# Kernel tuning notes

Hardware: AMD Instinct MI355X
Metric: run time of the kernel (lower is better)

The kernel has to match this reference:

```python
import jax, jax.numpy as jnp
import numpy as np

T, IN, H, OUT, L = 128, 64, 2048, 4096, 2  # steps, input_size, hidden, output vocab, layers


def lstm_cell(x, h, c, Wih, Whh, bih, bhh):
    # torch LSTMCell: gates = x W_ih^T + b_ih + h W_hh^T + b_hh; order i,f,g,o
    g = x @ Wih.T + bih + h @ Whh.T + bhh
    i, f, gg, o = jnp.split(g, 4, axis=-1)
    c_new = jax.nn.sigmoid(f) * c + jax.nn.sigmoid(i) * jnp.tanh(gg)
    h_new = jax.nn.sigmoid(o) * jnp.tanh(c_new)
    return h_new, c_new


def setup_inputs() -> dict:
    key = jax.random.key(0)
    ks = jax.random.split(key, 12)
    u = lambda k, shape, fan: jax.random.uniform(k, shape, jnp.float32, -1.0, 1.0) / np.sqrt(fan)
    return {
        "input": jax.random.normal(ks[0], (T, 1, IN), jnp.float32),
        "h0": jnp.zeros((L, 1, H), jnp.float32),
        "c0": jnp.zeros((L, 1, H), jnp.float32),
        "Wih0": u(ks[1], (4 * H, IN + 1), H),
        "Whh0": u(ks[2], (4 * H, H), H),
        "bih0": u(ks[3], (4 * H,), H),
        "bhh0": u(ks[4], (4 * H,), H),
        "Wih1": u(ks[5], (4 * H, H), H),
        "Whh1": u(ks[6], (4 * H, H), H),
        "bih1": u(ks[7], (4 * H,), H),
        "bhh1": u(ks[8], (4 * H,), H),
        "Wl": u(ks[9], (OUT, H), H),
        "bl": u(ks[10], (OUT,), H),
    }


def reference(input, h0, c0, Wih0, Whh0, bih0, bhh0, Wih1, Whh1, bih1, bhh1, Wl, bl):
    keys = jax.random.split(jax.random.key(42), input.shape[0])

    def step(carry, xs):
        prev, h, c = carry          # prev: [1,1] float (last sampled index, init 1.0)
        x_t, k = xs                 # x_t: [1, IN]
        xa = jnp.concatenate([prev, x_t], axis=1)  # [1, IN+1]
        h0n, c0n = lstm_cell(xa, h[0], c[0], Wih0, Whh0, bih0, bhh0)
        h1n, c1n = lstm_cell(h0n, h[1], c[1], Wih1, Whh1, bih1, bhh1)
        logits = h1n @ Wl.T + bl                    # [1, OUT]
        probs = jax.nn.softmax(logits, axis=-1)
        samp = jax.random.categorical(k, logits, axis=-1)  # multinomial(probs) == categorical(logits)
        prev_new = samp[:, None].astype(jnp.float32)       # fed back detached (int sample)
        return (prev_new, jnp.stack([h0n, h1n]), jnp.stack([c0n, c1n])), (samp, probs)

    init = (jnp.ones((1, 1), jnp.float32), h0, c0)
    _, (samples, probs) = jax.lax.scan(step, init, (input, keys))
    return samples, probs  # samples: [T,1] int, probs: [T,1,OUT]
```

## Files before the change

kernel.cpp:

```cpp
#include <hip/hip_runtime.h>
#include <cstdint>

#define TT 128
#define INW 64
#define HH 2048
#define OUTW 4096
#define NBLK 512
#define NTHR 256

typedef _Float16 half8 __attribute__((ext_vector_type(8)));

#define QSCALE 5747.3639f
#define DSCALE (1.0f / QSCALE)
#define QA 127.0f
#define DS2 (DSCALE / 127.0f)

#define P_BASE 32768
#define WS_NEED ((32768ull + 6144ull) * 4ull)

__device__ __forceinline__ float ld_sys(const float* p) {
  return __hip_atomic_load((const float*)p, __ATOMIC_RELAXED, __HIP_MEMORY_SCOPE_SYSTEM);
}
__device__ __forceinline__ void st_sys(float* p, float v) {
  __hip_atomic_store(p, v, __ATOMIC_RELAXED, __HIP_MEMORY_SCOPE_SYSTEM);
}
__device__ __forceinline__ void st_sys_u32(uint32_t* p, uint32_t v) {
  __hip_atomic_store(p, v, __ATOMIC_RELAXED, __HIP_MEMORY_SCOPE_SYSTEM);
}
__device__ __forceinline__ uint64_t ld_sys_u64(const uint64_t* p) {
  return __hip_atomic_load(p, __ATOMIC_RELAXED, __HIP_MEMORY_SCOPE_SYSTEM);
}
__device__ __forceinline__ void st_sys_u64(uint64_t* p, uint64_t v) {
  __hip_atomic_store(p, v, __ATOMIC_RELAXED, __HIP_MEMORY_SCOPE_SYSTEM);
}

__device__ __forceinline__ uint32_t poll_hi32(const uint64_t* p, uint32_t tag) {
  for (;;) {
    uint64_t v = ld_sys_u64(p);
    if ((uint32_t)(v >> 32) == tag) return (uint32_t)v;
    __builtin_amdgcn_s_sleep(1);
  }
}
__device__ __forceinline__ uint64_t poll_tag12(const uint64_t* p, uint32_t tag) {
  for (;;) {
    uint64_t v = ld_sys_u64(p);
    if ((uint32_t)(v >> 44) == tag) return v;
    __builtin_amdgcn_s_sleep(1);
  }
}

__device__ __forceinline__ uint32_t rotl32(uint32_t x, int r) {
  return (x << r) | (x >> (32 - r));
}

#define TF_ROUND(r) do { x0 += x1; x1 = rotl32(x1, r); x1 ^= x0; } while (0)

__device__ __forceinline__ void threefry2x32(uint32_t k0, uint32_t k1,
                                             uint32_t c0, uint32_t c1,
                                             uint32_t& o0, uint32_t& o1) {
  uint32_t ks2 = k0 ^ k1 ^ 0x1BD11BDAu;
  uint32_t x0 = c0 + k0;
  uint32_t x1 = c1 + k1;
  TF_ROUND(13); TF_ROUND(15); TF_ROUND(26); TF_ROUND(6);
  x0 += k1;  x1 += ks2 + 1u;
  TF_ROUND(17); TF_ROUND(29); TF_ROUND(16); TF_ROUND(24);
  x0 += ks2; x1 += k0 + 2u;
  TF_ROUND(13); TF_ROUND(15); TF_ROUND(26); TF_ROUND(6);
  x0 += k0;  x1 += k1 + 3u;
  TF_ROUND(17); TF_ROUND(29); TF_ROUND(16); TF_ROUND(24);
  x0 += k1;  x1 += ks2 + 4u;
  TF_ROUND(13); TF_ROUND(15); TF_ROUND(26); TF_ROUND(6);
  x0 += ks2; x1 += k0 + 5u;
  o0 = x0; o1 = x1;
}

__device__ __forceinline__ void step_key(int t, uint32_t& k0, uint32_t& k1) {
  threefry2x32(0u, 42u, 0u, (uint32_t)t, k0, k1);
}

__device__ __forceinline__ float gumbel_for(uint32_t k0, uint32_t k1, int j) {
  uint32_t o0, o1;
  threefry2x32(k0, k1, 0u, (uint32_t)j, o0, o1);
  uint32_t bits = o0 ^ o1;
  uint32_t fb = (bits >> 9) | 0x3f800000u;
  float f = __uint_as_float(fb) - 1.0f;
  float u = fmaxf(f, 1.1754943508222875e-38f);
  return -logf(-logf(u));
}

__device__ __forceinline__ float wave_sum(float v) {
  v += __shfl_xor(v, 1, 64);
  v += __shfl_xor(v, 2, 64);
  v += __shfl_xor(v, 4, 64);
  v += __shfl_xor(v, 8, 64);
  v += __shfl_xor(v, 16, 64);
  v += __shfl_xor(v, 32, 64);
  return v;
}

__device__ __forceinline__ float sigf(float x) { return 1.0f / (1.0f + expf(-x)); }

__device__ __forceinline__ float4 combine2(float4 a, float4 b) {
  float M = fmaxf(a.x, b.x);
  float S = a.y * expf(a.x - M) + b.y * expf(b.x - M);
  float g, w;
  if (b.z > a.z) { g = b.z; w = b.w; } else { g = a.z; w = a.w; }
  return make_float4(M, S, g, w);
}

__device__ __forceinline__ float dot8(half8 a, float4 v0, float4 v1) {
  return (float)a[0] * v0.x + (float)a[1] * v0.y + (float)a[2] * v0.z +
         (float)a[3] * v0.w + (float)a[4] * v1.x + (float)a[5] * v1.y +
         (float)a[6] * v1.z + (float)a[7] * v1.w;
}

__device__ __forceinline__ int dot4i_sw(uint32_t a, uint32_t b) {
  int s = 0;
#pragma unroll
  for (int k = 0; k < 4; ++k) {
    int av = ((int)(a << (24 - 8 * k))) >> 24;
    int bv = ((int)(b << (24 - 8 * k))) >> 24;
    s += av * bv;
  }
  return s;
}

__device__ __forceinline__ int dot8i(uint2 w, int x0, int x1, int acc) {
#if __has_builtin(__builtin_amdgcn_sdot4)
  acc = __builtin_amdgcn_sdot4((int)w.x, x0, acc, false);
  acc = __builtin_amdgcn_sdot4((int)w.y, x1, acc, false);
#else
  acc += dot4i_sw(w.x, (uint32_t)x0) + dot4i_sw(w.y, (uint32_t)x1);
#endif
  return acc;
}

__device__ __forceinline__ int q8(float x) {
  int q = (int)rintf(x * QSCALE);
  return min(127, max(-127, q));
}
__device__ __forceinline__ int q8a(float x) {
  int q = (int)rintf(x * QA);
  return min(127, max(-127, q));
}

__device__ __forceinline__ uint32_t pack4w(float4 a) {
  return (uint32_t)(q8(a.x) & 255) | ((uint32_t)(q8(a.y) & 255) << 8) |
         ((uint32_t)(q8(a.z) & 255) << 16) | ((uint32_t)(q8(a.w) & 255) << 24);
}
__device__ __forceinline__ uint2 pack8w(float4 a, float4 b) {
  return make_uint2(pack4w(a), pack4w(b));
}

__device__ __forceinline__ uint64_t pack8a(float4 a, float4 b) {
  uint32_t lo = (uint32_t)(q8a(a.x) & 255) | ((uint32_t)(q8a(a.y) & 255) << 8) |
                ((uint32_t)(q8a(a.z) & 255) << 16) | ((uint32_t)(q8a(a.w) & 255) << 24);
  uint32_t hi = (uint32_t)(q8a(b.x) & 255) | ((uint32_t)(q8a(b.y) & 255) << 8) |
                ((uint32_t)(q8a(b.z) & 255) << 16) | ((uint32_t)(q8a(b.w) & 255) << 24);
  return (uint64_t)lo | ((uint64_t)hi << 32);
}

__device__ __forceinline__ float4 mk_part(uint64_t w1, uint64_t w2) {
  return make_float4(__uint_as_float((uint32_t)w1),
                     __uint_as_float((uint32_t)(w1 >> 32)),
                     __uint_as_float((uint32_t)w2),
                     __int_as_float((int)((uint32_t)(w2 >> 32) & 0xFFFu)));
}

__global__ __launch_bounds__(256) void k_init(const float* __restrict__ h0i,
                                              const float* __restrict__ c0i,
                                              float* __restrict__ ws) {
  int i = blockIdx.x * 256 + threadIdx.x;
  ws[i] = h0i[i];
  ws[4096 + i] = h0i[2048 + i];
  ws[8192 + i] = c0i[i];
  ws[10240 + i] = c0i[2048 + i];
  uint32_t* pc = (uint32_t*)(ws + P_BASE);
  for (int k = i; k < 6144; k += 2048) st_sys_u32(&pc[k], 0u);
}

__global__ __launch_bounds__(256, 2) void k_persist(
    const float* __restrict__ input,
    const float* __restrict__ h0i, const float* __restrict__ c0i,
    const float* __restrict__ Wih0,
    const float* __restrict__ Whh0f,
    const float* __restrict__ Wih1f,
    const float* __restrict__ Whh1f,
    const float* __restrict__ Wlf,
    const float* __restrict__ bih0, const float* __restrict__ bhh0,
    const float* __restrict__ bih1, const float* __restrict__ bhh1,
    const float* __restrict__ bl,
    float* ws, float* __restrict__ out) {
  __shared__ __align__(16) float hA[HH];
  __shared__ half8 wlds[2048];
  __shared__ uint64_t xq64[256];
  __shared__ uint64_t hq64[256];
  __shared__ float4 wred[4];
  __shared__ float xa[64];
  __shared__ float lv[8];
  __shared__ float gv[8];
  __shared__ uint32_t kk[2];
  __shared__ int hb[4];

  uint64_t* h0w  = (uint64_t*)(ws + P_BASE);
  uint64_t* h1w  = (uint64_t*)(ws + P_BASE + 1024);
  float*    h1buf = ws + P_BASE + 2048;
  uint64_t* pw1  = (uint64_t*)(ws + P_BASE + 4096);
  uint64_t* pw2  = (uint64_t*)(ws + P_BASE + 5120);

  const int tid = threadIdx.x;
  const int b = blockIdx.x;
  const int wave = tid >> 6, lane = tid & 63;
  const int j = b * 4 + wave;

  float cA = c0i[j];
  float cB = c0i[2048 + j];

  uint2 w0r[4][4], wi1r[4][4], wh1r[4][4];
#pragma unroll
  for (int g = 0; g < 4; ++g) {
    const float4* r0 = (const float4*)(Whh0f + (size_t)(g * HH + j) * HH);
    const float4* ri = (const float4*)(Wih1f + (size_t)(g * HH + j) * HH);
    const float4* rh = (const float4*)(Whh1f + (size_t)(g * HH + j) * HH);
#pragma unroll
    for (int s = 0; s < 4; ++s) {
      w0r[g][s]  = pack8w(r0[s * 128 + lane], r0[s * 128 + 64 + lane]);
      wi1r[g][s] = pack8w(ri[s * 128 + lane], ri[s * 128 + 64 + lane]);
      wh1r[g][s] = pack8w(rh[s * 128 + lane], rh[s * 128 + 64 + lane]);
    }
  }
  float wx[4], wp[4], bs0[4], bs1[4];
#pragma unroll
  for (int g = 0; g < 4; ++g) {
    wx[g] = Wih0[(size_t)(g * HH + j) * 65 + 1 + lane];
    wp[g] = Wih0[(size_t)(g * HH + j) * 65];
    bs0[g] = bih0[g * HH + j] + bhh0[g * HH + j];
    bs1[g] = bih1[g * HH + j] + bhh1[g * HH + j];
  }
  float blv0 = bl[b * 8 + wave * 2];
  float blv1 = bl[b * 8 + wave * 2 + 1];

  for (int c = tid; c < 2048; c += 256) {
    int rl = c >> 8, q = c & 255, s = q >> 6, l = q & 63;
    const float4* s4 = (const float4*)(Wlf + (size_t)(b * 8 + rl) * HH);
    float4 a = s4[s * 128 + l];
    float4 bb = s4[s * 128 + 64 + l];
    half8 h;
    h[0] = (_Float16)a.x;  h[1] = (_Float16)a.y;
    h[2] = (_Float16)a.z;  h[3] = (_Float16)a.w;
    h[4] = (_Float16)bb.x; h[5] = (_Float16)bb.y;
    h[6] = (_Float16)bb.z; h[7] = (_Float16)bb.w;
    wlds[c] = h;
  }

  float lgr0 = 0.f, lgr1 = 0.f;

  for (int t = 0; t < TT; ++t) {
    if (tid < 64) xa[tid] = input[t * INW + tid];
    if (t == 0) {
      const float4* s4 = (const float4*)h0i;
      xq64[tid] = pack8a(s4[2 * tid], s4[2 * tid + 1]);
    }
    __syncthreads();
    int i0 = 0, i1 = 0, i2 = 0, i3 = 0;
    {
      const int* xi = (const int*)xq64;
#pragma unroll
      for (int s = 0; s < 4; ++s) {
        int v0 = xi[s * 128 + lane];
        int v1 = xi[s * 128 + 64 + lane];
        i0 = dot8i(w0r[0][s], v0, v1, i0);
        i1 = dot8i(w0r[1][s], v0, v1, i1);
        i2 = dot8i(w0r[2][s], v0, v1, i2);
        i3 = dot8i(w0r[3][s], v0, v1, i3);
      }
    }
    float xl = xa[lane];
    float f0 = wave_sum((float)i0 * DS2 + wx[0] * xl);
    float f1 = wave_sum((float)i1 * DS2 + wx[1] * xl);
    float f2 = wave_sum((float)i2 * DS2 + wx[2] * xl);
    float f3 = wave_sum((float)i3 * DS2 + wx[3] * xl);

    float prev;
    if (t > 0) {
      uint64_t w2a = poll_tag12(&pw2[tid], (uint32_t)t);
      uint64_t w2b = poll_tag12(&pw2[tid + 256], (uint32_t)t);
      __asm__ volatile("" ::: "memory");
      uint64_t w1a = ld_sys_u64(&pw1[tid]);
      uint64_t w1b = ld_sys_u64(&pw1[tid + 256]);
      float4 val = combine2(mk_part(w1a, w2a), mk_part(w1b, w2b));
#pragma unroll
      for (int k = 1; k < 64; k <<= 1) {
        float4 o = make_float4(__shfl_xor(val.x, k, 64), __shfl_xor(val.y, k, 64),
                               __shfl_xor(val.z, k, 64), __shfl_xor(val.w, k, 64));
        val = combine2(val, o);
      }
      if (lane == 0) wred[wave] = val;
      __syncthreads();
      float4 r = combine2(combine2(wred[0], wred[1]), combine2(wred[2], wred[3]));
      int samp = __float_as_int(r.w);
      prev = (float)samp;
      if (lane == 0) {
        int jj = b * 8 + wave * 2;
        out[TT + (size_t)(t - 1) * OUTW + jj]     = expf(lgr0 - r.x) / r.y;
        out[TT + (size_t)(t - 1) * OUTW + jj + 1] = expf(lgr1 - r.x) / r.y;
      }
      if (b == 0 && tid == 0) out[t - 1] = (float)samp;
    } else {
      prev = 1.0f;
    }

    if (lane == 0) {
      float gi_ = f0 + wp[0] * prev + bs0[0];
      float gf_ = f1 + wp[1] * prev + bs0[1];
      float gg_ = f2 + wp[2] * prev + bs0[2];
      float go_ = f3 + wp[3] * prev + bs0[3];
      float cn = sigf(gf_) * cA + sigf(gi_) * tanhf(gg_);
      cA = cn;
      float h = sigf(go_) * tanhf(cn);
      hb[wave] = q8a(h) & 255;
    }
    __syncthreads();
    if (tid == 0) {
      uint32_t lo = (uint32_t)hb[0] | ((uint32_t)hb[1] << 8) |
                    ((uint32_t)hb[2] << 16) | ((uint32_t)hb[3] << 24);
      st_sys_u64(&h0w[b], (uint64_t)lo | ((uint64_t)(t + 1) << 32));
    }

    {
      uint32_t bx0 = poll_hi32(&h0w[tid], (uint32_t)(t + 1));
      uint32_t bx1 = poll_hi32(&h0w[tid + 256], (uint32_t)(t + 1));
      ((uint32_t*)xq64)[tid] = bx0;
      ((uint32_t*)xq64)[tid + 256] = bx1;
      if (t == 0) {
        const float4* s4 = (const float4*)(h0i + 2048);
        hq64[tid] = pack8a(s4[2 * tid], s4[2 * tid + 1]);
      }
      __syncthreads();

      int a0 = 0, a1 = 0, a2 = 0, a3 = 0;
      const int* xi = (const int*)xq64;
      const int* hi = (const int*)hq64;
#pragma unroll
      for (int s = 0; s < 4; ++s) {
        int xv0 = xi[s * 128 + lane], xv1 = xi[s * 128 + 64 + lane];
        int hv0 = hi[s * 128 + lane], hv1 = hi[s * 128 + 64 + lane];
        a0 = dot8i(wi1r[0][s], xv0, xv1, a0);
        a1 = dot8i(wi1r[1][s], xv0, xv1, a1);
        a2 = dot8i(wi1r[2][s], xv0, xv1, a2);
        a3 = dot8i(wi1r[3][s], xv0, xv1, a3);
        a0 = dot8i(wh1r[0][s], hv0, hv1, a0);
        a1 = dot8i(wh1r[1][s], hv0, hv1, a1);
        a2 = dot8i(wh1r[2][s], hv0, hv1, a2);
        a3 = dot8i(wh1r[3][s], hv0, hv1, a3);
      }
      float g0 = wave_sum((float)a0) * DS2;
      float g1 = wave_sum((float)a1) * DS2;
      float g2 = wave_sum((float)a2) * DS2;
      float g3 = wave_sum((float)a3) * DS2;
      if (lane == 0) {
        float gi_ = g0 + bs1[0];
        float gf_ = g1 + bs1[1];
        float gg_ = g2 + bs1[2];
        float go_ = g3 + bs1[3];
        float cn = sigf(gf_) * cB + sigf(gi_) * tanhf(gg_);
        cB = cn;
        float h = sigf(go_) * tanhf(cn);
        st_sys(&h1buf[j], h);
        hb[wave] = q8a(h) & 255;
      }
      __syncthreads();
      if (tid == 0) {
        uint32_t lo = (uint32_t)hb[0] | ((uint32_t)hb[1] << 8) |
                      ((uint32_t)hb[2] << 16) | ((uint32_t)hb[3] << 24);
        st_sys_u64(&h1w[b], (uint64_t)lo | ((uint64_t)(t + 1) << 32));
      }
    }

    {
      if (tid == 0) {
        uint32_t k0, k1;
        step_key(t, k0, k1);
        kk[0] = k0; kk[1] = k1;
      }
      uint32_t cx0 = poll_hi32(&h1w[tid], (uint32_t)(t + 1));
      uint32_t cx1 = poll_hi32(&h1w[tid + 256], (uint32_t)(t + 1));
      __asm__ volatile("" ::: "memory");
      ((uint32_t*)hq64)[tid] = cx0;
      ((uint32_t*)hq64)[tid + 256] = cx1;
#pragma unroll
      for (int k2 = 0; k2 < 8; ++k2)
        hA[tid + 256 * k2] = ld_sys(&h1buf[tid + 256 * k2]);
      __syncthreads();

      const float4* h4 = (const float4*)hA;
#pragma unroll
      for (int r = 0; r < 2; ++r) {
        int jl = wave * 2 + r;
        int jj = b * 8 + jl;
        const half8* wr = &wlds[jl * 256];
        float acc = 0.f;
#pragma unroll
        for (int s = 0; s < 4; ++s) {
          int idx = s * 64 + lane;
          acc += dot8(wr[idx], h4[s * 128 + lane], h4[s * 128 + 64 + lane]);
        }
        acc = wave_sum(acc) + (r == 0 ? blv0 : blv1);
        if (r == 0) lgr0 = acc; else lgr1 = acc;
        if (lane == 0) {
          lv[jl] = acc;
          gv[jl] = acc + gumbel_for(kk[0], kk[1], jj);
        }
      }
      __syncthreads();
      if (tid == 0) {
        float m = -INFINITY, s = 0.f, gm = -INFINITY;
        int gi = 0;
#pragma unroll
        for (int k = 0; k < 8; ++k) {
          float l = lv[k];
          float m2 = fmaxf(m, l);
          s = s * expf(m - m2) + expf(l - m2);
          m = m2;
          float g = gv[k];
          if (g > gm) { gm = g; gi = b * 8 + k; }
        }
        uint64_t w1 = (uint64_t)__float_as_uint(m) |
                      ((uint64_t)__float_as_uint(s) << 32);
        uint32_t hi2 = ((uint32_t)(t + 1) << 12) | (uint32_t)gi;
        uint64_t w2 = (uint64_t)__float_as_uint(gm) | ((uint64_t)hi2 << 32);
        st_sys_u64(&pw1[b], w1);
        __builtin_amdgcn_s_waitcnt(0);
        st_sys_u64(&pw2[b], w2);
      }
    }
  }

  {
    uint64_t w2a = poll_tag12(&pw2[tid], (uint32_t)TT);
    uint64_t w2b = poll_tag12(&pw2[tid + 256], (uint32_t)TT);
    __asm__ volatile("" ::: "memory");
    uint64_t w1a = ld_sys_u64(&pw1[tid]);
    uint64_t w1b = ld_sys_u64(&pw1[tid + 256]);
    float4 val = combine2(mk_part(w1a, w2a), mk_part(w1b, w2b));
#pragma unroll
    for (int k = 1; k < 64; k <<= 1) {
      float4 o = make_float4(__shfl_xor(val.x, k, 64), __shfl_xor(val.y, k, 64),
                             __shfl_xor(val.z, k, 64), __shfl_xor(val.w, k, 64));
      val = combine2(val, o);
    }
    if (lane == 0) wred[wave] = val;
    __syncthreads();
    float4 r = combine2(combine2(wred[0], wred[1]), combine2(wred[2], wred[3]));
    if (lane == 0) {
      int jj = b * 8 + wave * 2;
      out[TT + (size_t)(TT - 1) * OUTW + jj]     = expf(lgr0 - r.x) / r.y;
      out[TT + (size_t)(TT - 1) * OUTW + jj + 1] = expf(lgr1 - r.x) / r.y;
    }
    if (b == 0 && tid == 0) out[TT - 1] = (float)__float_as_int(r.w);
  }
}


__device__ __forceinline__ float4 ld_sys4(const float4* p) {
  const float* f = (const float*)p;
  return make_float4(ld_sys(f), ld_sys(f + 1), ld_sys(f + 2), ld_sys(f + 3));
}

__global__ __launch_bounds__(256) void k_layer0(
    const float* __restrict__ input,
    const float* __restrict__ Wih0, const float* __restrict__ Whh0,
    const float* __restrict__ bih0, const float* __restrict__ bhh0,
    float* __restrict__ ws, float* __restrict__ out, int t) {
  __shared__ float h0s[HH];
  __shared__ float xa[72];
  __shared__ float4 red[256];

  float* h0buf = ws;
  float* c0 = ws + 8192;
  float* logits = ws + 12288;
  float4* partials = (float4*)(ws + 16384);

  const float* h0_in = h0buf + (t & 1) * HH;
  float* h0_out = h0buf + ((t + 1) & 1) * HH;

  const int tid = threadIdx.x;
  const int b = blockIdx.x;

  float prev;
  if (t > 0) {
    red[tid] = partials[tid];
    __syncthreads();
    for (int off = 128; off > 0; off >>= 1) {
      if (tid < off) red[tid] = combine2(red[tid], red[tid + off]);
      __syncthreads();
    }
    float4 r = red[0];
    int samp = __float_as_int(r.w);
    prev = (float)samp;
    if (tid < 8) {
      int j = b * 8 + tid;
      out[TT + (size_t)(t - 1) * OUTW + j] = expf(logits[j] - r.x) / r.y;
    }
    if (b == 0 && tid == 0) out[t - 1] = (float)samp;
  } else {
    prev = 1.0f;
  }

  if (tid == 0) xa[0] = prev;
  if (tid >= 1 && tid <= 64) xa[tid] = input[t * INW + tid - 1];
  for (int k = 0; k < HH / 256; ++k) h0s[tid + 256 * k] = h0_in[tid + 256 * k];
  __syncthreads();

  const int wave = tid >> 6, lane = tid & 63;
  const int j = b * 4 + wave;

  float acc0 = 0.f, acc1 = 0.f, acc2 = 0.f, acc3 = 0.f;
  {
    float xl = xa[lane];
    acc0 += Wih0[(size_t)(0 * HH + j) * 65 + lane] * xl;
    acc1 += Wih0[(size_t)(1 * HH + j) * 65 + lane] * xl;
    acc2 += Wih0[(size_t)(2 * HH + j) * 65 + lane] * xl;
    acc3 += Wih0[(size_t)(3 * HH + j) * 65 + lane] * xl;
    if (lane == 0) {
      float xe = xa[64];
      acc0 += Wih0[(size_t)(0 * HH + j) * 65 + 64] * xe;
      acc1 += Wih0[(size_t)(1 * HH + j) * 65 + 64] * xe;
      acc2 += Wih0[(size_t)(2 * HH + j) * 65 + 64] * xe;
      acc3 += Wih0[(size_t)(3 * HH + j) * 65 + 64] * xe;
    }
  }
  const float4* h4 = (const float4*)h0s;
  const float4* w0 = (const float4*)(Whh0 + (size_t)(0 * HH + j) * HH);
  const float4* w1 = (const float4*)(Whh0 + (size_t)(1 * HH + j) * HH);
  const float4* w2 = (const float4*)(Whh0 + (size_t)(2 * HH + j) * HH);
  const float4* w3 = (const float4*)(Whh0 + (size_t)(3 * HH + j) * HH);
  for (int s = 0; s < HH / 256; ++s) {
    int e = s * 64 + lane;
    float4 hv = h4[e];
    float4 a = w0[e];
    float4 bb = w1[e];
    float4 cc = w2[e];
    float4 dd = w3[e];
    acc0 += a.x * hv.x + a.y * hv.y + a.z * hv.z + a.w * hv.w;
    acc1 += bb.x * hv.x + bb.y * hv.y + bb.z * hv.z + bb.w * hv.w;
    acc2 += cc.x * hv.x + cc.y * hv.y + cc.z * hv.z + cc.w * hv.w;
    acc3 += dd.x * hv.x + dd.y * hv.y + dd.z * hv.z + dd.w * hv.w;
  }
  acc0 = wave_sum(acc0);
  acc1 = wave_sum(acc1);
  acc2 = wave_sum(acc2);
  acc3 = wave_sum(acc3);
  if (lane == 0) {
    float gi_ = acc0 + bih0[0 * HH + j] + bhh0[0 * HH + j];
    float gf_ = acc1 + bih0[1 * HH + j] + bhh0[1 * HH + j];
    float gg_ = acc2 + bih0[2 * HH + j] + bhh0[2 * HH + j];
    float go_ = acc3 + bih0[3 * HH + j] + bhh0[3 * HH + j];
    float c = c0[j];
    float cn = sigf(gf_) * c + sigf(gi_) * tanhf(gg_);
    c0[j] = cn;
    h0_out[j] = sigf(go_) * tanhf(cn);
  }
}

__global__ __launch_bounds__(256) void k_layer1(
    const float* __restrict__ Wih1, const float* __restrict__ Whh1,
    const float* __restrict__ bih1, const float* __restrict__ bhh1,
    float* __restrict__ ws, int t) {
  __shared__ float xs[HH];
  __shared__ float hs[HH];
  float* h0buf = ws;
  float* h1buf = ws + 4096;
  float* c1 = ws + 10240;
  const float* x_in = h0buf + ((t + 1) & 1) * HH;
  const float* h_in = h1buf + (t & 1) * HH;
  float* h_out = h1buf + ((t + 1) & 1) * HH;

  const int tid = threadIdx.x;
  const int b = blockIdx.x;
  for (int k = 0; k < HH / 256; ++k) {
    xs[tid + 256 * k] = x_in[tid + 256 * k];
    hs[tid + 256 * k] = h_in[tid + 256 * k];
  }
  __syncthreads();

  const int wave = tid >> 6, lane = tid & 63;
  const int j = b * 4 + wave;

  float acc0 = 0.f, acc1 = 0.f, acc2 = 0.f, acc3 = 0.f;
  const float4* x4 = (const float4*)xs;
  const float4* h4 = (const float4*)hs;
  const float4* wi0 = (const float4*)(Wih1 + (size_t)(0 * HH + j) * HH);
  const float4* wi1 = (const float4*)(Wih1 + (size_t)(1 * HH + j) * HH);
  const float4* wi2 = (const float4*)(Wih1 + (size_t)(2 * HH + j) * HH);
  const float4* wi3 = (const float4*)(Wih1 + (size_t)(3 * HH + j) * HH);
  const float4* wh0 = (const float4*)(Whh1 + (size_t)(0 * HH + j) * HH);
  const float4* wh1 = (const float4*)(Whh1 + (size_t)(1 * HH + j) * HH);
  const float4* wh2 = (const float4*)(Whh1 + (size_t)(2 * HH + j) * HH);
  const float4* wh3 = (const float4*)(Whh1 + (size_t)(3 * HH + j) * HH);
  for (int s = 0; s < HH / 256; ++s) {
    int e = s * 64 + lane;
    float4 xv = x4[e];
    float4 hv = h4[e];
    float4 a, bb;
    a = wi0[e]; acc0 += a.x * xv.x + a.y * xv.y + a.z * xv.z + a.w * xv.w;
    a = wi1[e]; acc1 += a.x * xv.x + a.y * xv.y + a.z * xv.z + a.w * xv.w;
    a = wi2[e]; acc2 += a.x * xv.x + a.y * xv.y + a.z * xv.z + a.w * xv.w;
    a = wi3[e]; acc3 += a.x * xv.x + a.y * xv.y + a.z * xv.z + a.w * xv.w;
    bb = wh0[e]; acc0 += bb.x * hv.x + bb.y * hv.y + bb.z * hv.z + bb.w * hv.w;
    bb = wh1[e]; acc1 += bb.x * hv.x + bb.y * hv.y + bb.z * hv.z + bb.w * hv.w;
    bb = wh2[e]; acc2 += bb.x * hv.x + bb.y * hv.y + bb.z * hv.z + bb.w * hv.w;
    bb = wh3[e]; acc3 += bb.x * hv.x + bb.y * hv.y + bb.z * hv.z + bb.w * hv.w;
  }
  acc0 = wave_sum(acc0);
  acc1 = wave_sum(acc1);
  acc2 = wave_sum(acc2);
  acc3 = wave_sum(acc3);
  if (lane == 0) {
    float gi_ = acc0 + bih1[0 * HH + j] + bhh1[0 * HH + j];
    float gf_ = acc1 + bih1[1 * HH + j] + bhh1[1 * HH + j];
    float gg_ = acc2 + bih1[2 * HH + j] + bhh1[2 * HH + j];
    float go_ = acc3 + bih1[3 * HH + j] + bhh1[3 * HH + j];
    float c = c1[j];
    float cn = sigf(gf_) * c + sigf(gi_) * tanhf(gg_);
    c1[j] = cn;
    h_out[j] = sigf(go_) * tanhf(cn);
  }
}

__global__ __launch_bounds__(256) void k_logits(
    const float* __restrict__ Wl, const float* __restrict__ bl,
    float* __restrict__ ws, int t) {
  __shared__ float hs[HH];
  __shared__ float lv[16];
  __shared__ float gv[16];
  __shared__ uint32_t kk[2];

  float* h1buf = ws + 4096;
  const float* h1n = h1buf + ((t + 1) & 1) * HH;
  float* logits = ws + 12288;
  float4* partials = (float4*)(ws + 16384);

  const int tid = threadIdx.x;
  const int b = blockIdx.x;
  if (tid == 0) {
    uint32_t k0, k1;
    step_key(t, k0, k1);
    kk[0] = k0; kk[1] = k1;
  }
  for (int k = 0; k < HH / 256; ++k) hs[tid + 256 * k] = h1n[tid + 256 * k];
  __syncthreads();

  const int wave = tid >> 6, lane = tid & 63;
  const float4* h4 = (const float4*)hs;
  for (int q = 0; q < 4; ++q) {
    int jl = wave * 4 + q;
    int j = b * 16 + jl;
    const float4* wr = (const float4*)(Wl + (size_t)j * HH);
    float acc = 0.f;
    for (int s = 0; s < HH / 256; ++s) {
      int e = s * 64 + lane;
      float4 w = wr[e];
      float4 h = h4[e];
      acc += w.x * h.x + w.y * h.y + w.z * h.z + w.w * h.w;
    }
    acc = wave_sum(acc);
    if (lane == 0) {
      float l = acc + bl[j];
      logits[j] = l;
      lv[jl] = l;
      gv[jl] = l + gumbel_for(kk[0], kk[1], j);
    }
  }
  __syncthreads();
  if (tid == 0) {
    float m = -INFINITY, s = 0.f, gm = -INFINITY;
    int gi = 0;
    for (int k = 0; k < 16; ++k) {
      float l = lv[k];
      float m2 = fmaxf(m, l);
      s = s * expf(m - m2) + expf(l - m2);
      m = m2;
      float g = gv[k];
      if (g > gm) { gm = g; gi = b * 16 + k; }
    }
    partials[b] = make_float4(m, s, gm, __int_as_float(gi));
  }
}

__global__ __launch_bounds__(256) void k_final(float* __restrict__ ws,
                                               float* __restrict__ out) {
  __shared__ float4 red[256];
  float* logits = ws + 12288;
  float4* partials = (float4*)(ws + 16384);
  const int tid = threadIdx.x;
  const int b = blockIdx.x;
  red[tid] = partials[tid];
  __syncthreads();
  for (int off = 128; off > 0; off >>= 1) {
    if (tid < off) red[tid] = combine2(red[tid], red[tid + off]);
    __syncthreads();
  }
  float4 r = red[0];
  if (tid < 16) {
    int j = b * 16 + tid;
    out[TT + (size_t)(TT - 1) * OUTW + j] = expf(logits[j] - r.x) / r.y;
  }
  if (b == 0 && tid == 0) out[TT - 1] = (float)__float_as_int(r.w);
}

extern "C" void kernel_launch(void* const* d_in, const int* in_sizes, int n_in,
                              void* d_out, int out_size, void* d_ws, size_t ws_size,
                              hipStream_t stream) {
  (void)in_sizes; (void)n_in; (void)out_size;
  const float* input = (const float*)d_in[0];
  const float* h0i  = (const float*)d_in[1];
  const float* c0i  = (const float*)d_in[2];
  const float* Wih0 = (const float*)d_in[3];
  const float* Whh0 = (const float*)d_in[4];
  const float* bih0 = (const float*)d_in[5];
  const float* bhh0 = (const float*)d_in[6];
  const float* Wih1 = (const float*)d_in[7];
  const float* Whh1 = (const float*)d_in[8];
  const float* bih1 = (const float*)d_in[9];
  const float* bhh1 = (const float*)d_in[10];
  const float* Wl   = (const float*)d_in[11];
  const float* bl   = (const float*)d_in[12];
  float* out = (float*)d_out;
  float* ws = (float*)d_ws;

  if (ws_size >= WS_NEED) {
    k_init<<<8, 256, 0, stream>>>(h0i, c0i, ws);
    k_persist<<<NBLK, NTHR, 0, stream>>>(input, h0i, c0i, Wih0,
                                         Whh0, Wih1, Whh1, Wl,
                                         bih0, bhh0, bih1, bhh1, bl,
                                         ws, out);
  } else {
    k_init<<<8, 256, 0, stream>>>(h0i, c0i, ws);
    for (int t = 0; t < TT; ++t) {
      k_layer0<<<512, 256, 0, stream>>>(input, Wih0, Whh0, bih0, bhh0, ws, out, t);
      k_layer1<<<512, 256, 0, stream>>>(Wih1, Whh1, bih1, bhh1, ws, t);
      k_logits<<<256, 256, 0, stream>>>(Wl, bl, ws, t);
    }
    k_final<<<256, 256, 0, stream>>>(ws, out);
  }
}
```

Before: 2.175 ms.

## Tag every cross-block word and overlap layer-1 recurrent dot with layer-0 wait

Reworks the persistent kernel's inter-block messaging. Every published word now carries its own step tag, so readers poll all words together instead of polling one flag and then doing dependent loads. The h1 vector is sent as fp16 plus int8 inside those tagged words, which drops the separate fp32 h1 buffer and the memory-ordering wait on the writer. The Whh1·h1 dot product is moved ahead of the wait for layer-0 h, so it overlaps the cross-block latency. A per-step __syncthreads is also removed by reading the input directly, and the cell math now runs on all lanes. The trade-off is more polling words per thread and fp16 precision for h1 in the output projection.

Measured after the change: 3.634 ms. 67.1% more time.

```diff
diff --git a/kernel.cpp b/kernel.cpp
--- a/kernel.cpp
+++ b/kernel.cpp
@@ -34,19 +34,12 @@
   __hip_atomic_store(p, v, __ATOMIC_RELAXED, __HIP_MEMORY_SCOPE_SYSTEM);
 }
 
-__device__ __forceinline__ uint32_t poll_hi32(const uint64_t* p, uint32_t tag) {
-  for (;;) {
-    uint64_t v = ld_sys_u64(p);
-    if ((uint32_t)(v >> 32) == tag) return (uint32_t)v;
-    __builtin_amdgcn_s_sleep(1);
-  }
-}
-__device__ __forceinline__ uint64_t poll_tag12(const uint64_t* p, uint32_t tag) {
-  for (;;) {
-    uint64_t v = ld_sys_u64(p);
-    if ((uint32_t)(v >> 44) == tag) return v;
-    __builtin_amdgcn_s_sleep(1);
-  }
+__device__ __forceinline__ uint64_t f2h64(float x) {
+  _Float16 h = (_Float16)x;
+  return (uint64_t)__builtin_bit_cast(uint16_t, h);
+}
+__device__ __forceinline__ float h2f(uint16_t u) {
+  return (float)__builtin_bit_cast(_Float16, u);
 }
 
 __device__ __forceinline__ uint32_t rotl32(uint32_t x, int r) {
@@ -160,13 +153,6 @@
   return (uint64_t)lo | ((uint64_t)hi << 32);
 }
 
-__device__ __forceinline__ float4 mk_part(uint64_t w1, uint64_t w2) {
-  return make_float4(__uint_as_float((uint32_t)w1),
-                     __uint_as_float((uint32_t)(w1 >> 32)),
-                     __uint_as_float((uint32_t)w2),
-                     __int_as_float((int)((uint32_t)(w2 >> 32) & 0xFFFu)));
-}
-
 __global__ __launch_bounds__(256) void k_init(const float* __restrict__ h0i,
                                               const float* __restrict__ c0i,
                                               float* __restrict__ ws) {
@@ -196,17 +182,15 @@
   __shared__ uint64_t xq64[256];
   __shared__ uint64_t hq64[256];
   __shared__ float4 wred[4];
-  __shared__ float xa[64];
   __shared__ float lv[8];
   __shared__ float gv[8];
   __shared__ uint32_t kk[2];
   __shared__ int hb[4];
-
-  uint64_t* h0w  = (uint64_t*)(ws + P_BASE);
-  uint64_t* h1w  = (uint64_t*)(ws + P_BASE + 1024);
-  float*    h1buf = ws + P_BASE + 2048;
-  uint64_t* pw1  = (uint64_t*)(ws + P_BASE + 4096);
-  uint64_t* pw2  = (uint64_t*)(ws + P_BASE + 5120);
+  __shared__ float hf[4];
+
+  uint64_t* h0w = (uint64_t*)(ws + P_BASE);
+  uint64_t* h1p = (uint64_t*)(ws + P_BASE + 1024);
+  uint64_t* pwp = (uint64_t*)(ws + P_BASE + 3072);
 
   const int tid = threadIdx.x;
   const int b = blockIdx.x;
@@ -256,12 +240,12 @@
   float lgr0 = 0.f, lgr1 = 0.f;
 
   for (int t = 0; t < TT; ++t) {
-    if (tid < 64) xa[tid] = input[t * INW + tid];
+    float xl = input[t * INW + lane];
     if (t == 0) {
       const float4* s4 = (const float4*)h0i;
       xq64[tid] = pack8a(s4[2 * tid], s4[2 * tid + 1]);
-    }
-    __syncthreads();
+      __syncthreads();
+    }
     int i0 = 0, i1 = 0, i2 = 0, i3 = 0;
     {
       const int* xi = (const int*)xq64;
@@ -275,7 +259,6 @@
         i3 = dot8i(w0r[3][s], v0, v1, i3);
       }
     }
-    float xl = xa[lane];
     float f0 = wave_sum((float)i0 * DS2 + wx[0] * xl);
     float f1 = wave_sum((float)i1 * DS2 + wx[1] * xl);
     float f2 = wave_sum((float)i2 * DS2 + wx[2] * xl);
@@ -283,12 +266,26 @@
 
     float prev;
     if (t > 0) {
-      uint64_t w2a = poll_tag12(&pw2[tid], (uint32_t)t);
-      uint64_t w2b = poll_tag12(&pw2[tid + 256], (uint32_t)t);
-      __asm__ volatile("" ::: "memory");
-      uint64_t w1a = ld_sys_u64(&pw1[tid]);
-      uint64_t w1b = ld_sys_u64(&pw1[tid + 256]);
-      float4 val = combine2(mk_part(w1a, w2a), mk_part(w1b, w2b));
+      uint32_t tg = (uint32_t)t;
+      const uint64_t* pp = pwp + 6 * tid;
+      uint64_t a0, a1, a2, b0, b1, b2;
+      for (;;) {
+        a0 = ld_sys_u64(pp);     a1 = ld_sys_u64(pp + 1); a2 = ld_sys_u64(pp + 2);
+        b0 = ld_sys_u64(pp + 3); b1 = ld_sys_u64(pp + 4); b2 = ld_sys_u64(pp + 5);
+        if (((uint32_t)(a0 >> 32) == tg) & ((uint32_t)(a1 >> 32) == tg) &
+            ((uint32_t)(a2 >> 44) == tg) & ((uint32_t)(b0 >> 32) == tg) &
+            ((uint32_t)(b1 >> 32) == tg) & ((uint32_t)(b2 >> 44) == tg)) break;
+        __builtin_amdgcn_s_sleep(1);
+      }
+      float4 pa = make_float4(__uint_as_float((uint32_t)a0),
+                              __uint_as_float((uint32_t)a1),
+                              __uint_as_float((uint32_t)a2),
+                              __int_as_float((int)((uint32_t)(a2 >> 32) & 0xFFFu)));
+      float4 pb = make_float4(__uint_as_float((uint32_t)b0),
+                              __uint_as_float((uint32_t)b1),
+                              __uint_as_float((uint32_t)b2),
+                              __int_as_float((int)((uint32_t)(b2 >> 32) & 0xFFFu)));
+      float4 val = combine2(pa, pb);
 #pragma unroll
       for (int k = 1; k < 64; k <<= 1) {
         float4 o = make_float4(__shfl_xor(val.x, k, 64), __shfl_xor(val.y, k, 64),
@@ -310,7 +307,7 @@
       prev = 1.0f;
     }
 
-    if (lane == 0) {
+    {
       float gi_ = f0 + wp[0] * prev + bs0[0];
       float gf_ = f1 + wp[1] * prev + bs0[1];
       float gg_ = f2 + wp[2] * prev + bs0[2];
@@ -318,7 +315,7 @@
       float cn = sigf(gf_) * cA + sigf(gi_) * tanhf(gg_);
       cA = cn;
       float h = sigf(go_) * tanhf(cn);
-      hb[wave] = q8a(h) & 255;
+      if (lane == 0) hb[wave] = q8a(h) & 255;
     }
     __syncthreads();
     if (tid == 0) {
@@ -328,37 +325,53 @@
     }
 
     {
-      uint32_t bx0 = poll_hi32(&h0w[tid], (uint32_t)(t + 1));
-      uint32_t bx1 = poll_hi32(&h0w[tid + 256], (uint32_t)(t + 1));
-      ((uint32_t*)xq64)[tid] = bx0;
-      ((uint32_t*)xq64)[tid + 256] = bx1;
       if (t == 0) {
         const float4* s4 = (const float4*)(h0i + 2048);
         hq64[tid] = pack8a(s4[2 * tid], s4[2 * tid + 1]);
+        __syncthreads();
+      }
+      int a0 = 0, a1 = 0, a2 = 0, a3 = 0;
+      {
+        const int* hi = (const int*)hq64;
+#pragma unroll
+        for (int s = 0; s < 4; ++s) {
+          int hv0 = hi[s * 128 + lane], hv1 = hi[s * 128 + 64 + lane];
+          a0 = dot8i(wh1r[0][s], hv0, hv1, a0);
+          a1 = dot8i(wh1r[1][s], hv0, hv1, a1);
+          a2 = dot8i(wh1r[2][s], hv0, hv1, a2);
+          a3 = dot8i(wh1r[3][s], hv0, hv1, a3);
+        }
+      }
+      {
+        uint32_t tg = (uint32_t)(t + 1);
+        const uint64_t* hp = h0w + 2 * tid;
+        uint64_t wa, wb;
+        for (;;) {
+          wa = ld_sys_u64(hp); wb = ld_sys_u64(hp + 1);
+          if (((uint32_t)(wa >> 32) == tg) & ((uint32_t)(wb >> 32) == tg)) break;
+          __builtin_amdgcn_s_sleep(1);
+        }
+        ((uint32_t*)xq64)[2 * tid]     = (uint32_t)wa;
+        ((uint32_t*)xq64)[2 * tid + 1] = (uint32_t)wb;
       }
       __syncthreads();
 
-      int a0 = 0, a1 = 0, a2 = 0, a3 = 0;
-      const int* xi = (const int*)xq64;
-      const int* hi = (const int*)hq64;
-#pragma unroll
-      for (int s = 0; s < 4; ++s) {
-        int xv0 = xi[s * 128 + lane], xv1 = xi[s * 128 + 64 + lane];
-        int hv0 = hi[s * 128 + lane], hv1 = hi[s * 128 + 64 + lane];
-        a0 = dot8i(wi1r[0][s], xv0, xv1, a0);
-        a1 = dot8i(wi1r[1][s], xv0, xv1, a1);
-        a2 = dot8i(wi1r[2][s], xv0, xv1, a2);
-        a3 = dot8i(wi1r[3][s], xv0, xv1, a3);
-        a0 = dot8i(wh1r[0][s], hv0, hv1, a0);
-        a1 = dot8i(wh1r[1][s], hv0, hv1, a1);
-        a2 = dot8i(wh1r[2][s], hv0, hv1, a2);
-        a3 = dot8i(wh1r[3][s], hv0, hv1, a3);
+      {
+        const int* xi = (const int*)xq64;
+#pragma unroll
+        for (int s = 0; s < 4; ++s) {
+          int xv0 = xi[s * 128 + lane], xv1 = xi[s * 128 + 64 + lane];
+          a0 = dot8i(wi1r[0][s], xv0, xv1, a0);
+          a1 = dot8i(wi1r[1][s], xv0, xv1, a1);
+          a2 = dot8i(wi1r[2][s], xv0, xv1, a2);
+          a3 = dot8i(wi1r[3][s], xv0, xv1, a3);
+        }
       }
       float g0 = wave_sum((float)a0) * DS2;
       float g1 = wave_sum((float)a1) * DS2;
       float g2 = wave_sum((float)a2) * DS2;
       float g3 = wave_sum((float)a3) * DS2;
-      if (lane == 0) {
+      {
         float gi_ = g0 + bs1[0];
         float gf_ = g1 + bs1[1];
         float gg_ = g2 + bs1[2];
@@ -366,14 +379,17 @@
         float cn = sigf(gf_) * cB + sigf(gi_) * tanhf(gg_);
         cB = cn;
         float h = sigf(go_) * tanhf(cn);
-        st_sys(&h1buf[j], h);
-        hb[wave] = q8a(h) & 255;
+        if (lane == 0) hf[wave] = h;
       }
       __syncthreads();
       if (tid == 0) {
-        uint32_t lo = (uint32_t)hb[0] | ((uint32_t)hb[1] << 8) |
-                      ((uint32_t)hb[2] << 16) | ((uint32_t)hb[3] << 24);
-        st_sys_u64(&h1w[b], (uint64_t)lo | ((uint64_t)(t + 1) << 32));
+        uint64_t tg = (uint64_t)(t + 1);
+        uint32_t i8 = (uint32_t)(q8a(hf[0]) & 255) | ((uint32_t)(q8a(hf[1]) & 255) << 8) |
+                      ((uint32_t)(q8a(hf[2]) & 255) << 16) | ((uint32_t)(q8a(hf[3]) & 255) << 24);
+        uint64_t w1 = f2h64(hf[0]) | (f2h64(hf[1]) << 16) | (f2h64(hf[2]) << 32) | (tg << 48);
+        uint64_t w2 = f2h64(hf[3]) | ((uint64_t)i8 << 16) | (tg << 48);
+        st_sys_u64(&h1p[2 * b], w1);
+        st_sys_u64(&h1p[2 * b + 1], w2);
       }
     }
 
@@ -383,14 +399,26 @@
         step_key(t, k0, k1);
         kk[0] = k0; kk[1] = k1;
       }
-      uint32_t cx0 = poll_hi32(&h1w[tid], (uint32_t)(t + 1));
-      uint32_t cx1 = poll_hi32(&h1w[tid + 256], (uint32_t)(t + 1));
-      __asm__ volatile("" ::: "memory");
-      ((uint32_t*)hq64)[tid] = cx0;
-      ((uint32_t*)hq64)[tid + 256] = cx1;
-#pragma unroll
-      for (int k2 = 0; k2 < 8; ++k2)
-        hA[tid + 256 * k2] = ld_sys(&h1buf[tid + 256 * k2]);
+      {
+        uint32_t tg = (uint32_t)(t + 1);
+        const uint64_t* qp = h1p + 4 * tid;
+        uint64_t w1a, w2a, w1b, w2b;
+        for (;;) {
+          w1a = ld_sys_u64(qp);     w2a = ld_sys_u64(qp + 1);
+          w1b = ld_sys_u64(qp + 2); w2b = ld_sys_u64(qp + 3);
+          if (((uint32_t)(w1a >> 48) == tg) & ((uint32_t)(w2a >> 48) == tg) &
+              ((uint32_t)(w1b >> 48) == tg) & ((uint32_t)(w2b >> 48) == tg)) break;
+          __builtin_amdgcn_s_sleep(1);
+        }
+        float4 fa = make_float4(h2f((uint16_t)w1a), h2f((uint16_t)(w1a >> 16)),
+                                h2f((uint16_t)(w1a >> 32)), h2f((uint16_t)w2a));
+        float4 fb = make_float4(h2f((uint16_t)w1b), h2f((uint16_t)(w1b >> 16)),
+                                h2f((uint16_t)(w1b >> 32)), h2f((uint16_t)w2b));
+        ((float4*)hA)[2 * tid]     = fa;
+        ((float4*)hA)[2 * tid + 1] = fb;
+        ((uint32_t*)hq64)[2 * tid]     = (uint32_t)(w2a >> 16);
+        ((uint32_t*)hq64)[2 * tid + 1] = (uint32_t)(w2b >> 16);
+      }
       __syncthreads();
 
       const float4* h4 = (const float4*)hA;
@@ -425,24 +453,36 @@
           float g = gv[k];
           if (g > gm) { gm = g; gi = b * 8 + k; }
         }
-        uint64_t w1 = (uint64_t)__float_as_uint(m) |
-                      ((uint64_t)__float_as_uint(s) << 32);
-        uint32_t hi2 = ((uint32_t)(t + 1) << 12) | (uint32_t)gi;
-        uint64_t w2 = (uint64_t)__float_as_uint(gm) | ((uint64_t)hi2 << 32);
-        st_sys_u64(&pw1[b], w1);
-        __builtin_amdgcn_s_waitcnt(0);
-        st_sys_u64(&pw2[b], w2);
+        uint64_t tg = (uint64_t)(t + 1);
+        st_sys_u64(&pwp[3 * b],     (uint64_t)__float_as_uint(m) | (tg << 32));
+        st_sys_u64(&pwp[3 * b + 1], (uint64_t)__float_as_uint(s) | (tg << 32));
+        st_sys_u64(&pwp[3 * b + 2], (uint64_t)__float_as_uint(gm) |
+                                    ((uint64_t)(((uint32_t)tg << 12) | (uint32_t)gi) << 32));
       }
     }
   }
 
   {
-    uint64_t w2a = poll_tag12(&pw2[tid], (uint32_t)TT);
-    uint64_t w2b = poll_tag12(&pw2[tid + 256], (uint32_t)TT);
-    __asm__ volatile("" ::: "memory");
-    uint64_t w1a = ld_sys_u64(&pw1[tid]);
-    uint64_t w1b = ld_sys_u64(&pw1[tid + 256]);
-    float4 val = combine2(mk_part(w1a, w2a), mk_part(w1b, w2b));
+    uint32_t tg = (uint32_t)TT;
+    const uint64_t* pp = pwp + 6 * tid;
+    uint64_t a0, a1, a2, b0, b1, b2;
+    for (;;) {
+      a0 = ld_sys_u64(pp);     a1 = ld_sys_u64(pp + 1); a2 = ld_sys_u64(pp + 2);
+      b0 = ld_sys_u64(pp + 3); b1 = ld_sys_u64(pp + 4); b2 = ld_sys_u64(pp + 5);
+      if (((uint32_t)(a0 >> 32) == tg) & ((uint32_t)(a1 >> 32) == tg) &
+          ((uint32_t)(a2 >> 44) == tg) & ((uint32_t)(b0 >> 32) == tg) &
+          ((uint32_t)(b1 >> 32) == tg) & ((uint32_t)(b2 >> 44) == tg)) break;
+      __builtin_amdgcn_s_sleep(1);
+    }
+    float4 pa = make_float4(__uint_as_float((uint32_t)a0),
+                            __uint_as_float((uint32_t)a1),
+                            __uint_as_float((uint32_t)a2),
+                            __int_as_float((int)((uint32_t)(a2 >> 32) & 0xFFFu)));
+    float4 pb = make_float4(__uint_as_float((uint32_t)b0),
+                            __uint_as_float((uint32_t)b1),
+                            __uint_as_float((uint32_t)b2),
+                            __int_as_float((int)((uint32_t)(b2 >> 32) & 0xFFFu)));
+    float4 val = combine2(pa, pb);
 #pragma unroll
     for (int k = 1; k < 64; k <<= 1) {
       float4 o = make_float4(__shfl_xor(val.x, k, 64), __shfl_xor(val.y, k, 64),
@@ -461,11 +501,6 @@
   }
 }
 
-
-__device__ __forceinline__ float4 ld_sys4(const float4* p) {
-  const float* f = (const float*)p;
-  return make_float4(ld_sys(f), ld_sys(f + 1), ld_sys(f + 2), ld_sys(f + 3));
-}
 
 __global__ __launch_bounds__(256) void k_layer0(
     const float* __restrict__ input,
```

## Overlap layer-1 recurrent dot with layer-0 wait and pack h1 as fp16

Applied to the files above, without the earlier changes.

Computes the layer-1 Whh·h contribution before polling for the layer-0 hidden flags, so that work overlaps the cross-block wait. The layer-1 hidden state is now published as packed fp16 values plus an int8-and-tag word, replacing the 8 scalar float system loads per thread with two 64-bit loads per thread. LSTM cell math is run by all lanes instead of lane 0 only, which removes divergence. The fp16 exchange of h1 for the logits adds a small precision loss.

Result: faster. 2.008 ms (-7.7%).

```diff
diff --git a/kernel.cpp b/kernel.cpp
--- a/kernel.cpp
+++ b/kernel.cpp
@@ -47,6 +47,14 @@
     if ((uint32_t)(v >> 44) == tag) return v;
     __builtin_amdgcn_s_sleep(1);
   }
+}
+
+__device__ __forceinline__ uint64_t f2h64(float x) {
+  _Float16 h = (_Float16)x;
+  return (uint64_t)__builtin_bit_cast(uint16_t, h);
+}
+__device__ __forceinline__ float h2f(uint16_t u) {
+  return (float)__builtin_bit_cast(_Float16, u);
 }
 
 __device__ __forceinline__ uint32_t rotl32(uint32_t x, int r) {
@@ -158,13 +166,6 @@
   uint32_t hi = (uint32_t)(q8a(b.x) & 255) | ((uint32_t)(q8a(b.y) & 255) << 8) |
                 ((uint32_t)(q8a(b.z) & 255) << 16) | ((uint32_t)(q8a(b.w) & 255) << 24);
   return (uint64_t)lo | ((uint64_t)hi << 32);
-}
-
-__device__ __forceinline__ float4 mk_part(uint64_t w1, uint64_t w2) {
-  return make_float4(__uint_as_float((uint32_t)w1),
-                     __uint_as_float((uint32_t)(w1 >> 32)),
-                     __uint_as_float((uint32_t)w2),
-                     __int_as_float((int)((uint32_t)(w2 >> 32) & 0xFFFu)));
 }
 
 __global__ __launch_bounds__(256) void k_init(const float* __restrict__ h0i,
@@ -201,12 +202,13 @@
   __shared__ float gv[8];
   __shared__ uint32_t kk[2];
   __shared__ int hb[4];
+  __shared__ float hf[4];
 
   uint64_t* h0w  = (uint64_t*)(ws + P_BASE);
-  uint64_t* h1w  = (uint64_t*)(ws + P_BASE + 1024);
-  float*    h1buf = ws + P_BASE + 2048;
-  uint64_t* pw1  = (uint64_t*)(ws + P_BASE + 4096);
-  uint64_t* pw2  = (uint64_t*)(ws + P_BASE + 5120);
+  uint64_t* h1p1 = (uint64_t*)(ws + P_BASE + 1024);
+  uint64_t* h1p2 = (uint64_t*)(ws + P_BASE + 2048);
+  uint64_t* pw1  = (uint64_t*)(ws + P_BASE + 3072);
+  uint64_t* pw2  = (uint64_t*)(ws + P_BASE + 4096);
 
   const int tid = threadIdx.x;
   const int b = blockIdx.x;
@@ -288,7 +290,15 @@
       __asm__ volatile("" ::: "memory");
       uint64_t w1a = ld_sys_u64(&pw1[tid]);
       uint64_t w1b = ld_sys_u64(&pw1[tid + 256]);
-      float4 val = combine2(mk_part(w1a, w2a), mk_part(w1b, w2b));
+      float4 pa = make_float4(__uint_as_float((uint32_t)w1a),
+                              __uint_as_float((uint32_t)(w1a >> 32)),
+                              __uint_as_float((uint32_t)w2a),
+                              __int_as_float((int)((uint32_t)(w2a >> 32) & 0xFFFu)));
+      float4 pb = make_float4(__uint_as_float((uint32_t)w1b),
+                              __uint_as_float((uint32_t)(w1b >> 32)),
+                              __uint_as_float((uint32_t)w2b),
+                              __int_as_float((int)((uint32_t)(w2b >> 32) & 0xFFFu)));
+      float4 val = combine2(pa, pb);
 #pragma unroll
       for (int k = 1; k < 64; k <<= 1) {
         float4 o = make_float4(__shfl_xor(val.x, k, 64), __shfl_xor(val.y, k, 64),
@@ -310,7 +320,7 @@
       prev = 1.0f;
     }
 
-    if (lane == 0) {
+    {
       float gi_ = f0 + wp[0] * prev + bs0[0];
       float gf_ = f1 + wp[1] * prev + bs0[1];
       float gg_ = f2 + wp[2] * prev + bs0[2];
@@ -318,7 +328,7 @@
       float cn = sigf(gf_) * cA + sigf(gi_) * tanhf(gg_);
       cA = cn;
       float h = sigf(go_) * tanhf(cn);
-      hb[wave] = q8a(h) & 255;
+      if (lane == 0) hb[wave] = q8a(h) & 255;
     }
     __syncthreads();
     if (tid == 0) {
@@ -328,37 +338,48 @@
     }
 
     {
-      uint32_t bx0 = poll_hi32(&h0w[tid], (uint32_t)(t + 1));
-      uint32_t bx1 = poll_hi32(&h0w[tid + 256], (uint32_t)(t + 1));
-      ((uint32_t*)xq64)[tid] = bx0;
-      ((uint32_t*)xq64)[tid + 256] = bx1;
       if (t == 0) {
         const float4* s4 = (const float4*)(h0i + 2048);
         hq64[tid] = pack8a(s4[2 * tid], s4[2 * tid + 1]);
+        __syncthreads();
+      }
+      int a0 = 0, a1 = 0, a2 = 0, a3 = 0;
+      {
+        const int* hi = (const int*)hq64;
+#pragma unroll
+        for (int s = 0; s < 4; ++s) {
+          int hv0 = hi[s * 128 + lane], hv1 = hi[s * 128 + 64 + lane];
+          a0 = dot8i(wh1r[0][s], hv0, hv1, a0);
+          a1 = dot8i(wh1r[1][s], hv0, hv1, a1);
+          a2 = dot8i(wh1r[2][s], hv0, hv1, a2);
+          a3 = dot8i(wh1r[3][s], hv0, hv1, a3);
+        }
+      }
+      {
+        uint32_t tg = (uint32_t)(t + 1);
+        uint32_t wa = poll_hi32(&h0w[tid], tg);
+        uint32_t wb = poll_hi32(&h0w[tid + 256], tg);
+        ((uint32_t*)xq64)[tid]       = wa;
+        ((uint32_t*)xq64)[tid + 256] = wb;
       }
       __syncthreads();
 
-      int a0 = 0, a1 = 0, a2 = 0, a3 = 0;
-      const int* xi = (const int*)xq64;
-      const int* hi = (const int*)hq64;
-#pragma unroll
-      for (int s = 0; s < 4; ++s) {
-        int xv0 = xi[s * 128 + lane], xv1 = xi[s * 128 + 64 + lane];
-        int hv0 = hi[s * 128 + lane], hv1 = hi[s * 128 + 64 + lane];
-        a0 = dot8i(wi1r[0][s], xv0, xv1, a0);
-        a1 = dot8i(wi1r[1][s], xv0, xv1, a1);
-        a2 = dot8i(wi1r[2][s], xv0, xv1, a2);
-        a3 = dot8i(wi1r[3][s], xv0, xv1, a3);
-        a0 = dot8i(wh1r[0][s], hv0, hv1, a0);
-        a1 = dot8i(wh1r[1][s], hv0, hv1, a1);
-        a2 = dot8i(wh1r[2][s], hv0, hv1, a2);
-        a3 = dot8i(wh1r[3][s], hv0, hv1, a3);
+      {
+        const int* xi = (const int*)xq64;
+#pragma unroll
+        for (int s = 0; s < 4; ++s) {
+          int xv0 = xi[s * 128 + lane], xv1 = xi[s * 128 + 64 + lane];
+          a0 = dot8i(wi1r[0][s], xv0, xv1, a0);
+          a1 = dot8i(wi1r[1][s], xv0, xv1, a1);
+          a2 = dot8i(wi1r[2][s], xv0, xv1, a2);
+          a3 = dot8i(wi1r[3][s], xv0, xv1, a3);
+        }
       }
       float g0 = wave_sum((float)a0) * DS2;
       float g1 = wave_sum((float)a1) * DS2;
       float g2 = wave_sum((float)a2) * DS2;
       float g3 = wave_sum((float)a3) * DS2;
-      if (lane == 0) {
+      {
         float gi_ = g0 + bs1[0];
         float gf_ = g1 + bs1[1];
         float gg_ = g2 + bs1[2];
@@ -366,14 +387,17 @@
         float cn = sigf(gf_) * cB + sigf(gi_) * tanhf(gg_);
         cB = cn;
         float h = sigf(go_) * tanhf(cn);
-        st_sys(&h1buf[j], h);
-        hb[wave] = q8a(h) & 255;
+        if (lane == 0) hf[wave] = h;
       }
       __syncthreads();
       if (tid == 0) {
-        uint32_t lo = (uint32_t)hb[0] | ((uint32_t)hb[1] << 8) |
-                      ((uint32_t)hb[2] << 16) | ((uint32_t)hb[3] << 24);
-        st_sys_u64(&h1w[b], (uint64_t)lo | ((uint64_t)(t + 1) << 32));
+        uint64_t w1 = f2h64(hf[0]) | (f2h64(hf[1]) << 16) |
+                      (f2h64(hf[2]) << 32) | (f2h64(hf[3]) << 48);
+        uint32_t i8 = (uint32_t)(q8a(hf[0]) & 255) | ((uint32_t)(q8a(hf[1]) & 255) << 8) |
+                      ((uint32_t)(q8a(hf[2]) & 255) << 16) | ((uint32_t)(q8a(hf[3]) & 255) << 24);
+        st_sys_u64(&h1p1[b], w1);
+        __builtin_amdgcn_s_waitcnt(0);
+        st_sys_u64(&h1p2[b], (uint64_t)i8 | ((uint64_t)(t + 1) << 32));
       }
     }
 
@@ -383,14 +407,22 @@
         step_key(t, k0, k1);
         kk[0] = k0; kk[1] = k1;
       }
-      uint32_t cx0 = poll_hi32(&h1w[tid], (uint32_t)(t + 1));
-      uint32_t cx1 = poll_hi32(&h1w[tid + 256], (uint32_t)(t + 1));
-      __asm__ volatile("" ::: "memory");
-      ((uint32_t*)hq64)[tid] = cx0;
-      ((uint32_t*)hq64)[tid + 256] = cx1;
-#pragma unroll
-      for (int k2 = 0; k2 < 8; ++k2)
-        hA[tid + 256 * k2] = ld_sys(&h1buf[tid + 256 * k2]);
+      {
+        uint32_t tg = (uint32_t)(t + 1);
+        uint32_t ia = poll_hi32(&h1p2[tid], tg);
+        uint32_t ib = poll_hi32(&h1p2[tid + 256], tg);
+        __asm__ volatile("" ::: "memory");
+        uint64_t w1a = ld_sys_u64(&h1p1[tid]);
+        uint64_t w1b = ld_sys_u64(&h1p1[tid + 256]);
+        float4 fa = make_float4(h2f((uint16_t)w1a), h2f((uint16_t)(w1a >> 16)),
+                                h2f((uint16_t)(w1a >> 32)), h2f((uint16_t)(w1a >> 48)));
+        float4 fb = make_float4(h2f((uint16_t)w1b), h2f((uint16_t)(w1b >> 16)),
+                                h2f((uint16_t)(w1b >> 32)), h2f((uint16_t)(w1b >> 48)));
+        ((float4*)hA)[tid]       = fa;
+        ((float4*)hA)[tid + 256] = fb;
+        ((uint32_t*)hq64)[tid]       = ia;
+        ((uint32_t*)hq64)[tid + 256] = ib;
+      }
       __syncthreads();
 
       const float4* h4 = (const float4*)hA;
@@ -442,7 +474,15 @@
     __asm__ volatile("" ::: "memory");
     uint64_t w1a = ld_sys_u64(&pw1[tid]);
     uint64_t w1b = ld_sys_u64(&pw1[tid + 256]);
-    float4 val = combine2(mk_part(w1a, w2a), mk_part(w1b, w2b));
+    float4 pa = make_float4(__uint_as_float((uint32_t)w1a),
+                            __uint_as_float((uint32_t)(w1a >> 32)),
+                            __uint_as_float((uint32_t)w2a),
+                            __int_as_float((int)((uint32_t)(w2a >> 32) & 0xFFFu)));
+    float4 pb = make_float4(__uint_as_float((uint32_t)w1b),
+                            __uint_as_float((uint32_t)(w1b >> 32)),
+                            __uint_as_float((uint32_t)w2b),
+                            __int_as_float((int)((uint32_t)(w2b >> 32) & 0xFFFu)));
+    float4 val = combine2(pa, pb);
 #pragma unroll
     for (int k = 1; k < 64; k <<= 1) {
       float4 o = make_float4(__shfl_xor(val.x, k, 64), __shfl_xor(val.y, k, 64),
@@ -461,11 +501,6 @@
   }
 }
 
-
-__device__ __forceinline__ float4 ld_sys4(const float4* p) {
-  const float* f = (const float*)p;
-  return make_float4(ld_sys(f), ld_sys(f + 1), ld_sys(f + 2), ld_sys(f + 3));
-}
 
 __global__ __launch_bounds__(256) void k_layer0(
     const float* __restrict__ input,
```
